# Optimization experiments

Hardware: AMD Instinct MI355X
Metric: run time of the kernel (lower is better)

## Reference

```python
import jax, jax.numpy as jnp
import numpy as np
from collections import deque

N, IN_DIM, H, B, L = 512, 64, 128, 256, 2
SOURCE = 105
E_UND = 2048


def _build_graph_and_masks():
    rng = np.random.default_rng(0)
    s = rng.integers(0, N, E_UND)
    d = rng.integers(0, N, E_UND)
    edge_index = np.stack([np.concatenate([s, d]), np.concatenate([d, s])]).astype(np.int32)
    # BFS depths from source (undirected)
    adj = [[] for _ in range(N)]
    for a, b in zip(edge_index[0], edge_index[1]):
        adj[int(a)].append(int(b))
    depths = np.full(N, np.inf)
    depths[SOURCE] = 0.0
    q = deque([SOURCE]); seen = {SOURCE}
    while q:
        u = q.popleft()
        for v in adj[u]:
            if v not in seen:
                seen.add(v); depths[v] = depths[u] + 1.0; q.append(v)
    finite = np.isfinite(depths)
    maxd = depths[finite].max() if finite.any() else 0.0
    depths[~finite] = maxd + 1.0
    adj_mask = np.zeros((N, N), np.float32)
    adj_mask[edge_index[0], edge_index[1]] = 1.0
    adj_mask[edge_index[1], edge_index[0]] = 1.0
    np.fill_diagonal(adj_mask, 1.0)
    direction_mask = (depths[None, :] <= depths[:, None]).astype(np.float32)
    # admittance_matrix is None -> uniform init, then masked
    initial_causal = (np.ones((N, N), np.float32) / N) * adj_mask * direction_mask
    return edge_index, adj_mask, direction_mask, initial_causal


def setup_inputs() -> dict:
    key = jax.random.key(0)
    ks = jax.random.split(key, 16)
    edge_index, adj_mask, direction_mask, initial_causal = _build_graph_and_masks()
    w = lambda k, shp: jax.random.normal(k, shp, jnp.float32) * 0.02
    return {
        'x': jax.random.normal(ks[0], (B, N, IN_DIM), jnp.float32),
        'edge_index': jnp.asarray(edge_index),
        'adj_mask': jnp.asarray(adj_mask),
        'direction_mask': jnp.asarray(direction_mask),
        'causal_logits': jnp.asarray(initial_causal),  # nn.Parameter init
        'W_in': w(ks[1], (IN_DIM, H)), 'b_in': jnp.zeros((H,), jnp.float32),
        'Wq': w(ks[2], (H, H)), 'bq': jnp.zeros((H,), jnp.float32),
        'Wk': w(ks[3], (H, H)), 'bk': jnp.zeros((H,), jnp.float32),
        'Wv': w(ks[4], (H, H)), 'bv': jnp.zeros((H,), jnp.float32),
        'gcn_W': w(ks[5], (L, H, H)), 'gcn_b': jnp.zeros((L, H), jnp.float32),
        'W_fuse': w(ks[6], (2 * H, H)), 'b_fuse': jnp.zeros((H,), jnp.float32),
        'ln_g': jnp.ones((H,), jnp.float32), 'ln_b': jnp.zeros((H,), jnp.float32),
    }


def reference(x, edge_index, adj_mask, direction_mask, causal_logits,
              W_in, b_in, Wq, bq, Wk, bk, Wv, bv,
              gcn_W, gcn_b, W_fuse, b_fuse, ln_g, ln_b):
    n = adj_mask.shape[0]
    h = jax.nn.relu(x @ W_in + b_in)                               # (B,N,H)

    # causal matrix: softmax over learned logits, physically masked, renormalized
    C = jax.nn.softmax(causal_logits, axis=-1) * adj_mask * direction_mask
    C = C / jnp.clip(C.sum(-1, keepdims=True), 1e-8)

    # masked causal attention
    Q = h @ Wq + bq; K = h @ Wk + bk; V = h @ Wv + bv
    scale = jnp.asarray(h.shape[-1] ** 0.5, h.dtype)
    attn = jax.nn.softmax(jnp.einsum('bnh,bmh->bnm', Q, K) / scale, axis=-1)
    attn = attn * C[None]
    attn = attn / (attn.sum(-1, keepdims=True) + 1e-8)
    h_causal = jnp.einsum('bnm,bmh->bnh', attn, V)

    # GCNConv stack (self-loops + symmetric norm; dropout is identity in eval)
    src = jnp.concatenate([edge_index[0], jnp.arange(n, dtype=edge_index.dtype)])
    dst = jnp.concatenate([edge_index[1], jnp.arange(n, dtype=edge_index.dtype)])
    deg = jnp.zeros((n,), h.dtype).at[dst].add(1.0)
    dinv = deg ** -0.5                                              # deg>=1 (self loops)
    norm = (dinv[src] * dinv[dst])[None, :, None]                   # (1,E+N,1)
    h_g = h
    for l in range(gcn_W.shape[0]):
        hW = h_g @ gcn_W[l]                                         # (B,N,H)
        msg = hW[:, src, :] * norm                                  # (B,E+N,H)
        h_g = jnp.zeros_like(hW).at[:, dst, :].add(msg) + gcn_b[l]
        h_g = jax.nn.relu(h_g)

    h_comb = jnp.concatenate([h_causal, h_g], axis=-1) @ W_fuse + b_fuse
    mu = h_comb.mean(-1, keepdims=True)
    var = ((h_comb - mu) ** 2).mean(-1, keepdims=True)
    out = (h_comb - mu) / jnp.sqrt(var + 1e-5) * ln_g + ln_b
    return out, C
```

## Files before the change

kernel.cpp:

```cpp
#include <hip/hip_runtime.h>
#include <hip/hip_bf16.h>
#include <math.h>

#define NN 512
#define HH 128
#define INDIM 64
#define BB 256
#define NE 4096
#define MROWS (BB*NN)
#define OUT0 (BB*NN*HH)

typedef __attribute__((ext_vector_type(8))) short short8v;
typedef __attribute__((ext_vector_type(4))) float float4v;

__device__ __forceinline__ unsigned short f2bf(float f) {
  unsigned u = __float_as_uint(f);
  unsigned r = (u + 0x7fffu + ((u >> 16) & 1u)) >> 16;
  return (unsigned short)r;
}
__device__ __forceinline__ float bf2f(unsigned short b) {
  return __uint_as_float(((unsigned)b) << 16);
}

__global__ __launch_bounds__(256) void k_causalC(
    const float* __restrict__ logits, const float* __restrict__ adj,
    const float* __restrict__ dir, float* __restrict__ Cout)
{
  const int row = blockIdx.x;
  const int t = threadIdx.x;
  __shared__ float red[256];
  const float* lrow = logits + (size_t)row * NN;
  float v0 = lrow[t], v1 = lrow[t + 256];
  float mx = fmaxf(v0, v1);
  red[t] = mx; __syncthreads();
  for (int s = 128; s > 0; s >>= 1) { if (t < s) red[t] = fmaxf(red[t], red[t + s]); __syncthreads(); }
  mx = red[0]; __syncthreads();
  float e0 = __expf(v0 - mx), e1 = __expf(v1 - mx);
  red[t] = e0 + e1; __syncthreads();
  for (int s = 128; s > 0; s >>= 1) { if (t < s) red[t] += red[t + s]; __syncthreads(); }
  float sumE = red[0]; __syncthreads();
  float m0 = adj[(size_t)row * NN + t] * dir[(size_t)row * NN + t];
  float m1 = adj[(size_t)row * NN + t + 256] * dir[(size_t)row * NN + t + 256];
  float me0 = e0 * m0, me1 = e1 * m1;
  red[t] = me0 + me1; __syncthreads();
  for (int s = 128; s > 0; s >>= 1) { if (t < s) red[t] += red[t + s]; __syncthreads(); }
  float sumME = red[0];
  float sm = sumME / sumE;
  float denom = fmaxf(sm, 1e-8f) * sumE;
  Cout[(size_t)row * NN + t]       = me0 / denom;
  Cout[(size_t)row * NN + t + 256] = me1 / denom;
}

__global__ __launch_bounds__(512) void k_csr(const int* __restrict__ ei,
                                             int* __restrict__ rp,
                                             int* __restrict__ ci,
                                             float* __restrict__ cw)
{
  __shared__ int scnt[512];
  __shared__ float sdinv[512];
  __shared__ int sval[512];
  __shared__ int scur[512];
  const int t = threadIdx.x;
  const int* src = ei;
  const int* dst = ei + NE;
  scnt[t] = 0;
  __syncthreads();
  for (int e = t; e < NE; e += 512) atomicAdd(&scnt[dst[e]], 1);
  __syncthreads();
  const int deg = scnt[t] + 1;
  sdinv[t] = rsqrtf((float)deg);
  sval[t] = deg;
  __syncthreads();
  for (int off = 1; off < 512; off <<= 1) {
    int add = (t >= off) ? sval[t - off] : 0;
    __syncthreads();
    sval[t] += add;
    __syncthreads();
  }
  const int excl = sval[t] - deg;
  rp[t] = excl;
  if (t == 511) rp[512] = excl + deg;
  ci[excl] = t;
  cw[excl] = sdinv[t] * sdinv[t];
  scur[t] = excl + 1;
  __syncthreads();
  for (int e = t; e < NE; e += 512) {
    int s = src[e], d = dst[e];
    int p = atomicAdd(&scur[d], 1);
    ci[p] = s;
    cw[p] = sdinv[s] * sdinv[d];
  }
}

__global__ __launch_bounds__(512) void k_ccsr(const int* __restrict__ ei,
                                              const float* __restrict__ Cmat,
                                              int* __restrict__ rp,
                                              int* __restrict__ ci,
                                              float* __restrict__ cw)
{
  __shared__ unsigned bm[512 * 16];
  __shared__ int cnt[512];
  __shared__ int sval[512];
  __shared__ int cur[512];
  const int t = threadIdx.x;
  const int* src = ei;
  const int* dst = ei + NE;
  for (int i = t; i < 512 * 16; i += 512) bm[i] = 0u;
  __syncthreads();
  bm[t * 16 + (t >> 5)] |= (1u << (t & 31));
  cnt[t] = 1;
  __syncthreads();
  for (int e = t; e < NE; e += 512) {
    int r = src[e], c = dst[e];
    if (Cmat[(size_t)r * NN + c] > 0.f) {
      unsigned bit = 1u << (c & 31);
      unsigned old = atomicOr(&bm[r * 16 + (c >> 5)], bit);
      if (!(old & bit)) atomicAdd(&cnt[r], 1);
    }
  }
  __syncthreads();
  const int myc = cnt[t];
  sval[t] = myc;
  __syncthreads();
  for (int off = 1; off < 512; off <<= 1) {
    int add = (t >= off) ? sval[t - off] : 0;
    __syncthreads();
    sval[t] += add;
    __syncthreads();
  }
  const int excl = sval[t] - myc;
  rp[t] = excl;
  if (t == 511) rp[512] = excl + myc;
  ci[excl] = t;
  cw[excl] = Cmat[(size_t)t * NN + t];
  cur[t] = excl + 1;
  bm[t * 16 + (t >> 5)] &= ~(1u << (t & 31));
  __syncthreads();
  for (int e = t; e < NE; e += 512) {
    int r = src[e], c = dst[e];
    if (Cmat[(size_t)r * NN + c] > 0.f) {
      unsigned bit = 1u << (c & 31);
      unsigned old = atomicAnd(&bm[r * 16 + (c >> 5)], ~bit);
      if (old & bit) {
        int p = atomicAdd(&cur[r], 1);
        ci[p] = c;
        cw[p] = Cmat[(size_t)r * NN + c];
      }
    }
  }
}

__device__ __forceinline__ void gcn_body(
    int bid, const unsigned short* __restrict__ hW,
    const int* __restrict__ rp, const int* __restrict__ ci,
    const float* __restrict__ cw, const float* __restrict__ bias,
    unsigned short* __restrict__ out, int OS, int OC0)
{
  const int i5 = bid >> 3;
  const int ng = i5 & 31;
  const int b = (bid & 7) * 32 + (i5 >> 5);
  const int t = threadIdx.x;
  const int node = ng * 16 + (t >> 4);
  const int f0 = (t & 15) * 8;

  float bcol[8];
  #pragma unroll
  for (int k = 0; k < 8; k++) bcol[k] = bias[f0 + k];

  const unsigned short* base = hW + (size_t)b * 512 * 128;
  const int beg = rp[node], end = rp[node + 1];
  float acc[8] = {0.f, 0.f, 0.f, 0.f, 0.f, 0.f, 0.f, 0.f};
  for (int j = beg; j < end; j++) {
    int s = ci[j];
    float w = cw[j];
    short8v v = *(const short8v*)&base[(size_t)s * 128 + f0];
    #pragma unroll
    for (int k = 0; k < 8; k++) acc[k] += w * bf2f((unsigned short)v[k]);
  }
  short8v o;
  #pragma unroll
  for (int k = 0; k < 8; k++) {
    float v = fmaxf(acc[k] + bcol[k], 0.f);
    o[k] = (short)f2bf(v);
  }
  *(short8v*)&out[((size_t)(b * 512 + node)) * OS + OC0 + f0] = o;
}

__global__ __launch_bounds__(256) void k_gcn(
    const unsigned short* __restrict__ hW,
    const int* __restrict__ rp, const int* __restrict__ ci,
    const float* __restrict__ cw, const float* __restrict__ bias,
    unsigned short* __restrict__ out, int OS, int OC0)
{
  gcn_body(blockIdx.x, hW, rp, ci, cw, bias, out, OS, OC0);
}

__device__ __forceinline__ void sattn_body(
    int bid, const unsigned short* __restrict__ Qbf,
    const unsigned short* __restrict__ Kbf, const unsigned short* __restrict__ Vbf,
    const int* __restrict__ rp, const int* __restrict__ ci,
    const float* __restrict__ cw, unsigned short* __restrict__ Ocb)
{
  const int i5 = bid >> 3;
  const int ng = i5 & 31;
  const int b = (bid & 7) * 32 + (i5 >> 5);
  const int t = threadIdx.x;
  const int node = ng * 16 + (t >> 4);
  const int f0 = (t & 15) * 8;
  const float scale = 0.088388347648318447f;

  const size_t rowq = ((size_t)(b * 512 + node)) * 128 + f0;
  short8v qv = *(const short8v*)&Qbf[rowq];
  float qf[8];
  #pragma unroll
  for (int k = 0; k < 8; k++) qf[k] = bf2f((unsigned short)qv[k]);

  const unsigned short* Kb = Kbf + (size_t)b * 512 * 128;
  const unsigned short* Vb = Vbf + (size_t)b * 512 * 128;
  const int beg = rp[node], end = rp[node + 1];
  float acc[8] = {0.f, 0.f, 0.f, 0.f, 0.f, 0.f, 0.f, 0.f};
  float sw = 0.f;
  int j = beg;
  float w0 = cw[j];
  int m = ci[j];
  short8v kv = *(const short8v*)&Kb[(size_t)m * 128 + f0];
  short8v vv = *(const short8v*)&Vb[(size_t)m * 128 + f0];
  for (; j < end; ) {
    const int jn = (j + 1 < end) ? j + 1 : j;
    const float w02 = cw[jn];
    const int m2 = ci[jn];
    short8v kv2 = *(const short8v*)&Kb[(size_t)m2 * 128 + f0];
    short8v vv2 = *(const short8v*)&Vb[(size_t)m2 * 128 + f0];
    float part = 0.f;
    #pragma unroll
    for (int k = 0; k < 8; k++) part += qf[k] * bf2f((unsigned short)kv[k]);
    part += __shfl_xor(part, 1);
    part += __shfl_xor(part, 2);
    part += __shfl_xor(part, 4);
    part += __shfl_xor(part, 8);
    float w = __expf(part * scale) * w0;
    sw += w;
    #pragma unroll
    for (int k = 0; k < 8; k++) acc[k] += w * bf2f((unsigned short)vv[k]);
    j++;
    w0 = w02; kv = kv2; vv = vv2;
  }
  float inv = 1.0f / sw;
  short8v o;
  #pragma unroll
  for (int k = 0; k < 8; k++) o[k] = (short)f2bf(acc[k] * inv);
  *(short8v*)&Ocb[((size_t)(b * 512 + node)) * 256 + f0] = o;
}

__global__ __launch_bounds__(256) void k_gs(
    const unsigned short* __restrict__ hW,
    const int* __restrict__ grp, const int* __restrict__ gci,
    const float* __restrict__ gcw, const float* __restrict__ gbias,
    const unsigned short* __restrict__ Qbf, const unsigned short* __restrict__ Kbf,
    const unsigned short* __restrict__ Vbf,
    const int* __restrict__ arp, const int* __restrict__ aci,
    const float* __restrict__ acw,
    unsigned short* __restrict__ Dout)
{
  if (blockIdx.x < 8192)
    gcn_body(blockIdx.x, hW, grp, gci, gcw, gbias, Dout, 256, 128);
  else
    sattn_body(blockIdx.x - 8192, Qbf, Kbf, Vbf, arp, aci, acw, Dout);
}

__global__ __launch_bounds__(256) void k_wt(
    const float* s0, const float* s1, const float* s2, const float* s3,
    const float* s4, const float* s5, const float* s6,
    unsigned short* d0, unsigned short* d1, unsigned short* d2, unsigned short* d3,
    unsigned short* d4, unsigned short* d5, unsigned short* d6)
{
  const float* srcs[7] = {s0, s1, s2, s3, s4, s5, s6};
  unsigned short* dsts[7] = {d0, d1, d2, d3, d4, d5, d6};
  const int Ks[7] = {64, 128, 128, 128, 128, 128, 256};
  const int j = blockIdx.x >> 3;
  const int nc = blockIdx.x & 7;
  const float* s = srcs[j];
  unsigned short* d = dsts[j];
  const int K = Ks[j];
  const int STRW = K + 8;
  const int n0 = nc * 16;
  __shared__ short tile[16 * 264];
  const int t = threadIdx.x;
  for (int i = t; i < K * 16; i += 256) {
    int k = i >> 4, nn = i & 15;
    tile[nn * STRW + k] = (short)f2bf(s[k * 128 + n0 + nn]);
  }
  __syncthreads();
  for (int i = t; i < K * 2; i += 256) {
    int nn = (i * 8) / K;
    int k  = (i * 8) % K;
    *(short8v*)&d[(size_t)(n0 + nn) * K + k] =
        *(const short8v*)&tile[nn * STRW + k];
  }
}

template<bool RELU>
__global__ __launch_bounds__(256) void k_wgemm(
    const unsigned short* __restrict__ Abf,
    const unsigned short* __restrict__ Wt,
    const float* __restrict__ bias,
    unsigned short* __restrict__ Out)
{
  constexpr int STR = 136;
  __shared__ short Ws[128 * STR];
  __shared__ short rep[4 * 2048];
  const int t = threadIdx.x;
  const int wave = t >> 6, lane = t & 63;
  const int l15 = lane & 15, quad = lane >> 4;
  short* rw = rep + wave * 2048;

  for (int i = t; i < 128 * 16; i += 256) {
    int n = i >> 4, seg = i & 15;
    *(short8v*)&Ws[n * STR + seg * 8] =
        *(const short8v*)&Wt[(size_t)n * 128 + seg * 8];
  }
  float bcol[8];
  #pragma unroll
  for (int nt = 0; nt < 8; nt++) bcol[nt] = bias ? bias[nt * 16 + l15] : 0.f;
  __syncthreads();

  const int nwaves = gridDim.x * 4;
  int tile = blockIdx.x * 4 + wave;
  short8v af[4], afn[4];
  if (tile < MROWS / 16) {
    #pragma unroll
    for (int dc = 0; dc < 4; dc++)
      af[dc] = *(const short8v*)&Abf[((size_t)(tile * 16 + l15)) * 128 + dc * 32 + quad * 8];
  }
  while (tile < MROWS / 16) {
    const int ntile = tile + nwaves;
    if (ntile < MROWS / 16) {
      #pragma unroll
      for (int dc = 0; dc < 4; dc++)
        afn[dc] = *(const short8v*)&Abf[((size_t)(ntile * 16 + l15)) * 128 + dc * 32 + quad * 8];
    }
    float4v acc[8];
    #pragma unroll
    for (int nt = 0; nt < 8; nt++) acc[nt] = (float4v){0.f, 0.f, 0.f, 0.f};
    #pragma unroll
    for (int k32 = 0; k32 < 4; k32++) {
      #pragma unroll
      for (int nt = 0; nt < 8; nt++) {
        short8v wf = *(const short8v*)&Ws[(nt * 16 + l15) * STR + k32 * 32 + quad * 8];
        acc[nt] = __builtin_amdgcn_mfma_f32_16x16x32_bf16(af[k32], wf, acc[nt], 0, 0, 0);
      }
    }
    #pragma unroll
    for (int nt = 0; nt < 8; nt++)
      #pragma unroll
      for (int r = 0; r < 4; r++) {
        float v = acc[nt][r] + bcol[nt];
        if (RELU) v = fmaxf(v, 0.f);
        rw[(quad * 4 + r) * 128 + nt * 16 + l15] = (short)f2bf(v);
      }
    asm volatile("s_waitcnt lgkmcnt(0)" ::: "memory");
    __builtin_amdgcn_sched_barrier(0);
    #pragma unroll
    for (int p = 0; p < 4; p++) {
      int row16 = (lane >> 4) + p * 4, seg = lane & 15;
      short8v vv = *(const short8v*)&rw[row16 * 128 + seg * 8];
      *(short8v*)&Out[((size_t)(tile * 16 + row16)) * 128 + seg * 8] = vv;
    }
    tile = ntile;
    #pragma unroll
    for (int dc = 0; dc < 4; dc++) af[dc] = afn[dc];
  }
}

#define GNT 4
template<int KD, bool RELU, bool BATCHW, int OMODE, bool AF32>
__global__ __launch_bounds__(256) void k_bgemm(
    const void* __restrict__ Ap, const unsigned short* __restrict__ Wt,
    const float* __restrict__ bias, void* __restrict__ Out, int OS,
    const float* __restrict__ lng, const float* __restrict__ lnb)
{
  constexpr int KCH = (KD < 128) ? KD : 128;
  constexpr int STR = KCH + 8;
  constexpr bool WONCE = (KD <= 128);
  constexpr int ASH = (64 * STR > 8192) ? 64 * STR : 8192;
  constexpr int TRIPS = KCH / 32;
  __shared__ short lds[ASH + 128 * STR];
  short* As = lds;
  short* Ws = lds + ASH;
  const unsigned short* Abf = (const unsigned short*)Ap;
  const float* Af = (const float*)Ap;
  const int t = threadIdx.x;
  const int wave = t >> 6, lane = t & 63;
  const int l15 = lane & 15, quad = lane >> 4;

  short8v ap[TRIPS];
  float4 fa[TRIPS], fb[TRIPS];

  auto LOADC = [&](int rb, int kc) {
    #pragma unroll
    for (int j = 0; j < TRIPS; j++) {
      int i = t + j * 256;
      int r = i / (KCH / 8), seg = i % (KCH / 8);
      if (AF32) {
        const float* sp = &Af[(size_t)(rb + r) * KD + kc + seg * 8];
        fa[j] = *(const float4*)sp;
        fb[j] = *(const float4*)(sp + 4);
      } else {
        int arow = BATCHW ? ((rb & 511) + r) : (rb + r);
        ap[j] = *(const short8v*)&Abf[(size_t)arow * KD + kc + seg * 8];
      }
    }
  };
  auto STOREC = [&]() {
    #pragma unroll
    for (int j = 0; j < TRIPS; j++) {
      int i = t + j * 256;
      int r = i / (KCH / 8), seg = i % (KCH / 8);
      if (AF32) {
        short8v pk;
        pk[0] = (short)f2bf(fa[j].x); pk[1] = (short)f2bf(fa[j].y);
        pk[2] = (short)f2bf(fa[j].z); pk[3] = (short)f2bf(fa[j].w);
        pk[4] = (short)f2bf(fb[j].x); pk[5] = (short)f2bf(fb[j].y);
        pk[6] = (short)f2bf(fb[j].z); pk[7] = (short)f2bf(fb[j].w);
        *(short8v*)&As[r * STR + seg * 8] = pk;
      } else {
        *(short8v*)&As[r * STR + seg * 8] = ap[j];
      }
    }
  };

  float bcol[8];
  #pragma unroll
  for (int nt = 0; nt < 8; nt++) bcol[nt] = bias ? bias[nt * 16 + l15] : 0.f;
  float gcol[8], bbcol[8];
  if (OMODE == 2) {
    #pragma unroll
    for (int nt = 0; nt < 8; nt++) { gcol[nt] = lng[nt * 16 + l15]; bbcol[nt] = lnb[nt * 16 + l15]; }
  }

  for (int g = blockIdx.x; g < (MROWS / 64) / GNT; g += gridDim.x) {
    if (WONCE) {
      const int b0 = (g * GNT * 64) >> 9;
      const unsigned short* Wb = BATCHW ? (Wt + (size_t)b0 * 128 * KD) : Wt;
      for (int i = t; i < 128 * (KCH / 8); i += 256) {
        int n = i / (KCH / 8), seg = i % (KCH / 8);
        *(short8v*)&Ws[n * STR + seg * 8] =
            *(const short8v*)&Wb[(size_t)n * KD + seg * 8];
      }
    }
    LOADC(g * GNT * 64, 0);
    for (int tt = 0; tt < GNT; tt++) {
      const int tile = g * GNT + tt;
      const int rowbase = tile * 64;
      const int b = rowbase >> 9;
      float4v acc[8];
      #pragma unroll
      for (int nt = 0; nt < 8; nt++) acc[nt] = (float4v){0.f, 0.f, 0.f, 0.f};

      for (int kc = 0; kc < KD; kc += KCH) {
        __syncthreads();
        STOREC();
        if (!WONCE) {
          const unsigned short* Wb = BATCHW ? (Wt + (size_t)b * 128 * KD) : Wt;
          for (int i = t; i < 128 * (KCH / 8); i += 256) {
            int n = i / (KCH / 8), seg = i % (KCH / 8);
            *(short8v*)&Ws[n * STR + seg * 8] =
                *(const short8v*)&Wb[(size_t)n * KD + kc + seg * 8];
          }
        }
        __syncthreads();
        {
          int nkc = kc + KCH, ntt = tt;
          if (nkc >= KD) { nkc = 0; ntt = tt + 1; }
          if (ntt < GNT) LOADC((g * GNT + ntt) * 64, nkc);
        }
        #pragma unroll
        for (int k32 = 0; k32 < KCH / 32; k32++) {
          short8v af = *(const short8v*)&As[(wave * 16 + l15) * STR + k32 * 32 + quad * 8];
          #pragma unroll
          for (int nt = 0; nt < 8; nt++) {
            short8v wf = *(const short8v*)&Ws[(nt * 16 + l15) * STR + k32 * 32 + quad * 8];
            acc[nt] = __builtin_amdgcn_mfma_f32_16x16x32_bf16(af, wf, acc[nt], 0, 0, 0);
          }
        }
      }

      __syncthreads();
      if (OMODE == 0) {
        short* rep = As + wave * 2048;
        #pragma unroll
        for (int nt = 0; nt < 8; nt++)
          #pragma unroll
          for (int r = 0; r < 4; r++) {
            float v = acc[nt][r] + bcol[nt];
            if (RELU) v = fmaxf(v, 0.f);
            rep[(quad * 4 + r) * 128 + nt * 16 + l15] = (short)f2bf(v);
          }
        __syncthreads();
        unsigned short* Ob = (unsigned short*)Out;
        #pragma unroll
        for (int p = 0; p < 4; p++) {
          int row16 = (lane >> 4) + p * 4, seg = lane & 15;
          short8v vv = *(const short8v*)&rep[row16 * 128 + seg * 8];
          *(short8v*)&Ob[(size_t)(rowbase + wave * 16 + row16) * OS + seg * 8] = vv;
        }
      } else if (OMODE == 1) {
        short* rep = As + wave * 2048;
        #pragma unroll
        for (int nt = 0; nt < 8; nt++)
          #pragma unroll
          for (int r = 0; r < 4; r++) {
            float v = acc[nt][r] + bcol[nt];
            if (RELU) v = fmaxf(v, 0.f);
            rep[(nt * 16 + l15) * 16 + quad * 4 + r] = (short)f2bf(v);
          }
        __syncthreads();
        unsigned short* Ob = (unsigned short*)Out;
        int node0 = (rowbase & 511) + wave * 16;
        #pragma unroll
        for (int p = 0; p < 4; p++) {
          int idx = p * 64 + lane, c = idx >> 1, half = idx & 1;
          short8v vv = *(const short8v*)&rep[c * 16 + half * 8];
          *(short8v*)&Ob[((size_t)(b * 128 + c)) * 512 + node0 + half * 8] = vv;
        }
      } else {
        float* repw = (float*)lds + wave * 2048;
        float vv[8][4];
        float s[4] = {0, 0, 0, 0}, ss[4] = {0, 0, 0, 0};
        #pragma unroll
        for (int nt = 0; nt < 8; nt++)
          #pragma unroll
          for (int r = 0; r < 4; r++) {
            float v = acc[nt][r] + bcol[nt];
            vv[nt][r] = v;
            s[r] += v; ss[r] += v * v;
          }
        #pragma unroll
        for (int r = 0; r < 4; r++) {
          s[r] += __shfl_xor(s[r], 1);  s[r] += __shfl_xor(s[r], 2);
          s[r] += __shfl_xor(s[r], 4);  s[r] += __shfl_xor(s[r], 8);
          ss[r] += __shfl_xor(ss[r], 1); ss[r] += __shfl_xor(ss[r], 2);
          ss[r] += __shfl_xor(ss[r], 4); ss[r] += __shfl_xor(ss[r], 8);
        }
        #pragma unroll
        for (int r = 0; r < 4; r++) {
          float mu = s[r] * (1.0f / 128.0f);
          float var = ss[r] * (1.0f / 128.0f) - mu * mu;
          float inv = rsqrtf(var + 1e-5f);
          #pragma unroll
          for (int nt = 0; nt < 8; nt++)
            repw[(quad * 4 + r) * 128 + nt * 16 + l15] =
                (vv[nt][r] - mu) * inv * gcol[nt] + bbcol[nt];
        }
        __syncthreads();
        float* Of = (float*)Out;
        #pragma unroll
        for (int p = 0; p < 8; p++) {
          int row16 = (lane >> 5) + p * 2, seg = lane & 31;
          float4 o = *(const float4*)&repw[row16 * 128 + seg * 4];
          *(float4*)&Of[(size_t)(rowbase + wave * 16 + row16) * 128 + seg * 4] = o;
        }
      }
    }
  }
}

__global__ __launch_bounds__(256) void k_hqkv4(
    const float* __restrict__ x,
    const unsigned short* __restrict__ Wint,
    const float* __restrict__ bin,
    const unsigned short* __restrict__ W0, const unsigned short* __restrict__ W1,
    const unsigned short* __restrict__ W2, const unsigned short* __restrict__ W3,
    const float* __restrict__ b1, const float* __restrict__ b2,
    const float* __restrict__ b3,
    unsigned short* __restrict__ O0, unsigned short* __restrict__ O1,
    unsigned short* __restrict__ O2, unsigned short* __restrict__ O3)
{
  constexpr int STR = 136;
  constexpr int RSTR = 136;
  __shared__ short Ws[128 * STR];
  __shared__ short rep[4 * 2304];
  const int t = threadIdx.x;
  const int wave = t >> 6, lane = t & 63;
  const int l15 = lane & 15, quad = lane >> 4;
  short* rw = rep + wave * 2304;

  const unsigned short* Wsrc[4] = {W0, W1, W2, W3};
  const float* Bsrc[4] = {nullptr, b1, b2, b3};
  unsigned short* Osrc[4] = {O0, O1, O2, O3};

  float bh[8];
  #pragma unroll
  for (int nt = 0; nt < 8; nt++) bh[nt] = bin[nt * 16 + l15];

  for (int g = blockIdx.x; g < (MROWS / 64) / GNT; g += gridDim.x) {
    short8v wif[2][8];
    #pragma unroll
    for (int k32 = 0; k32 < 2; k32++)
      #pragma unroll
      for (int nt = 0; nt < 8; nt++)
        wif[k32][nt] = *(const short8v*)&Wint[(size_t)(nt * 16 + l15) * 64 + k32 * 32 + quad * 8];

    short8v af_all[GNT][4];
    #pragma unroll
    for (int tt = 0; tt < GNT; tt++) {
      const int row0 = (g * GNT + tt) * 64 + wave * 16;
      const float* xp = &x[(size_t)(row0 + l15) * 64 + quad * 16];
      float4 fx0 = *(const float4*)(xp);
      float4 fx1 = *(const float4*)(xp + 4);
      float4 fx2 = *(const float4*)(xp + 8);
      float4 fx3 = *(const float4*)(xp + 12);
      short8v px0, px1;
      px0[0] = (short)f2bf(fx0.x); px0[1] = (short)f2bf(fx0.y);
      px0[2] = (short)f2bf(fx0.z); px0[3] = (short)f2bf(fx0.w);
      px0[4] = (short)f2bf(fx1.x); px0[5] = (short)f2bf(fx1.y);
      px0[6] = (short)f2bf(fx1.z); px0[7] = (short)f2bf(fx1.w);
      px1[0] = (short)f2bf(fx2.x); px1[1] = (short)f2bf(fx2.y);
      px1[2] = (short)f2bf(fx2.z); px1[3] = (short)f2bf(fx2.w);
      px1[4] = (short)f2bf(fx3.x); px1[5] = (short)f2bf(fx3.y);
      px1[6] = (short)f2bf(fx3.z); px1[7] = (short)f2bf(fx3.w);
      *(short8v*)&rw[l15 * 72 + quad * 16]     = px0;
      *(short8v*)&rw[l15 * 72 + quad * 16 + 8] = px1;
      asm volatile("s_waitcnt lgkmcnt(0)" ::: "memory");
      __builtin_amdgcn_sched_barrier(0);

      float4v hacc[8];
      #pragma unroll
      for (int nt = 0; nt < 8; nt++) hacc[nt] = (float4v){0.f, 0.f, 0.f, 0.f};
      #pragma unroll
      for (int k32 = 0; k32 < 2; k32++) {
        short8v ax = *(const short8v*)&rw[l15 * 72 + k32 * 32 + quad * 8];
        #pragma unroll
        for (int nt = 0; nt < 8; nt++)
          hacc[nt] = __builtin_amdgcn_mfma_f32_16x16x32_bf16(ax, wif[k32][nt], hacc[nt], 0, 0, 0);
      }
      #pragma unroll
      for (int nt = 0; nt < 8; nt++)
        #pragma unroll
        for (int r = 0; r < 4; r++) {
          float v = fmaxf(hacc[nt][r] + bh[nt], 0.f);
          rw[(quad * 4 + r) * RSTR + nt * 16 + l15] = (short)f2bf(v);
        }
      asm volatile("s_waitcnt lgkmcnt(0)" ::: "memory");
      __builtin_amdgcn_sched_barrier(0);
      #pragma unroll
      for (int dc = 0; dc < 4; dc++)
        af_all[tt][dc] = *(const short8v*)&rw[l15 * RSTR + dc * 32 + quad * 8];
    }

    #pragma unroll
    for (int s = 0; s < 4; s++) {
      __syncthreads();
      for (int i = t; i < 128 * 16; i += 256) {
        int n = i >> 4, seg = i & 15;
        *(short8v*)&Ws[n * STR + seg * 8] =
            *(const short8v*)&Wsrc[s][(size_t)n * 128 + seg * 8];
      }
      float bcol[8];
      #pragma unroll
      for (int nt = 0; nt < 8; nt++) bcol[nt] = Bsrc[s] ? Bsrc[s][nt * 16 + l15] : 0.f;
      __syncthreads();

      #pragma unroll
      for (int tt = 0; tt < GNT; tt++) {
        const int rowbase = (g * GNT + tt) * 64;
        float4v acc[8];
        #pragma unroll
        for (int nt = 0; nt < 8; nt++) acc[nt] = (float4v){0.f, 0.f, 0.f, 0.f};
        #pragma unroll
        for (int k32 = 0; k32 < 4; k32++) {
          #pragma unroll
          for (int nt = 0; nt < 8; nt++) {
            short8v wf = *(const short8v*)&Ws[(nt * 16 + l15) * STR + k32 * 32 + quad * 8];
            acc[nt] = __builtin_amdgcn_mfma_f32_16x16x32_bf16(af_all[tt][k32], wf, acc[nt], 0, 0, 0);
          }
        }
        #pragma unroll
        for (int nt = 0; nt < 8; nt++)
          #pragma unroll
          for (int r = 0; r < 4; r++) {
            float v = acc[nt][r] + bcol[nt];
            rw[(quad * 4 + r) * RSTR + nt * 16 + l15] = (short)f2bf(v);
          }
        asm volatile("s_waitcnt lgkmcnt(0)" ::: "memory");
        __builtin_amdgcn_sched_barrier(0);
        unsigned short* Ob = Osrc[s];
        #pragma unroll
        for (int p = 0; p < 4; p++) {
          int row16 = (lane >> 4) + p * 4, seg = lane & 15;
          short8v vv = *(const short8v*)&rw[row16 * RSTR + seg * 8];
          *(short8v*)&Ob[(size_t)(rowbase + wave * 16 + row16) * 128 + seg * 8] = vv;
        }
      }
    }
  }
}

extern "C" void kernel_launch(void* const* d_in, const int* in_sizes, int n_in,
                              void* d_out, int out_size, void* d_ws, size_t ws_size,
                              hipStream_t stream)
{
  const float* x     = (const float*)d_in[0];
  const int*   ei    = (const int*)d_in[1];
  const float* adj   = (const float*)d_in[2];
  const float* dmask = (const float*)d_in[3];
  const float* clog  = (const float*)d_in[4];
  const float* W_in  = (const float*)d_in[5];
  const float* b_in  = (const float*)d_in[6];
  const float* Wq    = (const float*)d_in[7];
  const float* bq    = (const float*)d_in[8];
  const float* Wk    = (const float*)d_in[9];
  const float* bk    = (const float*)d_in[10];
  const float* Wv    = (const float*)d_in[11];
  const float* bv    = (const float*)d_in[12];
  const float* gcnW  = (const float*)d_in[13];
  const float* gcnB  = (const float*)d_in[14];
  const float* Wf    = (const float*)d_in[15];
  const float* bf    = (const float*)d_in[16];
  const float* lng   = (const float*)d_in[17];
  const float* lnb   = (const float*)d_in[18];

  float* outp = (float*)d_out;
  float* Cmat = outp + OUT0;

  char* W = (char*)d_ws;
  const size_t SLOT = (size_t)MROWS * 128 * 2;
  unsigned short* A0 = (unsigned short*)(W);
  unsigned short* B0 = (unsigned short*)(W + SLOT);
  unsigned short* C0 = (unsigned short*)(W + 2 * SLOT);
  unsigned short* D0 = (unsigned short*)(W + 3 * SLOT);
  char* AUX = W + 5 * SLOT;
  int*   csr_rp = (int*)AUX;
  int*   csr_ci = csr_rp + 640;
  float* csr_cw = (float*)(csr_ci + 4608);
  int*   crp    = (int*)(AUX + 131072);
  int*   cci    = crp + 640;
  float* ccw    = (float*)(cci + 8192);
  unsigned short* WB    = (unsigned short*)(AUX + 512 * 512 * 4) + 512 * 512 * 2;
  unsigned short* W_int = WB;
  unsigned short* Wqt   = WB + 8192;
  unsigned short* Wkt   = Wqt + 16384;
  unsigned short* Wvt   = Wkt + 16384;
  unsigned short* G0t   = Wvt + 16384;
  unsigned short* G1t   = G0t + 16384;
  unsigned short* Wft   = G1t + 16384;

  unsigned short* Vbf = (unsigned short*)outp;
  unsigned short* E0  = Vbf + (size_t)MROWS * 128;

  k_causalC<<<512, 256, 0, stream>>>(clog, adj, dmask, Cmat);
  k_csr<<<1, 512, 0, stream>>>(ei, csr_rp, csr_ci, csr_cw);
  k_ccsr<<<1, 512, 0, stream>>>(ei, Cmat, crp, cci, ccw);
  k_wt<<<56, 256, 0, stream>>>(W_in, Wq, Wk, Wv, gcnW, gcnW + HH * HH, Wf,
                               W_int, Wqt, Wkt, Wvt, G0t, G1t, Wft);

  k_hqkv4<<<512, 256, 0, stream>>>(
      x, W_int, b_in, G0t, Wqt, Wkt, Wvt, bq, bk, bv, A0, C0, E0, Vbf);
  k_gcn<<<8192, 256, 0, stream>>>(A0, csr_rp, csr_ci, csr_cw, gcnB, B0, 128, 0);
  k_wgemm<false><<<768, 256, 0, stream>>>(B0, G1t, nullptr, A0);
  k_gs<<<16384, 256, 0, stream>>>(
      A0, csr_rp, csr_ci, csr_cw, gcnB + HH,
      C0, E0, Vbf, crp, cci, ccw, D0);
  k_bgemm<256, false, false, 2, false><<<512, 256, 0, stream>>>(
      D0, Wft, bf, outp, 128, lng, lnb);
}
```

Before: 392.8 us.

## Use 512-thread blocks for hqkv4 and wgemm, stage W_in in LDS

```diff
diff --git a/kernel.cpp b/kernel.cpp
--- a/kernel.cpp
+++ b/kernel.cpp
@@ -300,7 +300,7 @@
 }
 
 template<bool RELU>
-__global__ __launch_bounds__(256) void k_wgemm(
+__global__ __launch_bounds__(512) void k_wgemm(
     const unsigned short* __restrict__ Abf,
     const unsigned short* __restrict__ Wt,
     const float* __restrict__ bias,
@@ -308,13 +308,13 @@
 {
   constexpr int STR = 136;
   __shared__ short Ws[128 * STR];
-  __shared__ short rep[4 * 2048];
+  __shared__ short rep[8 * 2048];
   const int t = threadIdx.x;
   const int wave = t >> 6, lane = t & 63;
   const int l15 = lane & 15, quad = lane >> 4;
   short* rw = rep + wave * 2048;
 
-  for (int i = t; i < 128 * 16; i += 256) {
+  for (int i = t; i < 128 * 16; i += 512) {
     int n = i >> 4, seg = i & 15;
     *(short8v*)&Ws[n * STR + seg * 8] =
         *(const short8v*)&Wt[(size_t)n * 128 + seg * 8];
@@ -324,8 +324,8 @@
   for (int nt = 0; nt < 8; nt++) bcol[nt] = bias ? bias[nt * 16 + l15] : 0.f;
   __syncthreads();
 
-  const int nwaves = gridDim.x * 4;
-  int tile = blockIdx.x * 4 + wave;
+  const int nwaves = gridDim.x * 8;
+  int tile = blockIdx.x * 8 + wave;
   short8v af[4], afn[4];
   if (tile < MROWS / 16) {
     #pragma unroll
@@ -565,7 +565,7 @@
   }
 }
 
-__global__ __launch_bounds__(256) void k_hqkv4(
+__global__ __launch_bounds__(512) void k_hqkv4(
     const float* __restrict__ x,
     const unsigned short* __restrict__ Wint,
     const float* __restrict__ bin,
@@ -579,7 +579,7 @@
   constexpr int STR = 136;
   constexpr int RSTR = 136;
   __shared__ short Ws[128 * STR];
-  __shared__ short rep[4 * 2304];
+  __shared__ short rep[8 * 2304];
   const int t = threadIdx.x;
   const int wave = t >> 6, lane = t & 63;
   const int l15 = lane & 15, quad = lane >> 4;
@@ -593,18 +593,19 @@
   #pragma unroll
   for (int nt = 0; nt < 8; nt++) bh[nt] = bin[nt * 16 + l15];
 
-  for (int g = blockIdx.x; g < (MROWS / 64) / GNT; g += gridDim.x) {
-    short8v wif[2][8];
-    #pragma unroll
-    for (int k32 = 0; k32 < 2; k32++)
-      #pragma unroll
-      for (int nt = 0; nt < 8; nt++)
-        wif[k32][nt] = *(const short8v*)&Wint[(size_t)(nt * 16 + l15) * 64 + k32 * 32 + quad * 8];
-
-    short8v af_all[GNT][4];
-    #pragma unroll
-    for (int tt = 0; tt < GNT; tt++) {
-      const int row0 = (g * GNT + tt) * 64 + wave * 16;
+  for (int g = blockIdx.x; g < MROWS / 256; g += gridDim.x) {
+    __syncthreads();
+    for (int i = t; i < 128 * 8; i += 512) {
+      int n = i >> 3, seg = i & 7;
+      *(short8v*)&Ws[n * STR + seg * 8] =
+          *(const short8v*)&Wint[(size_t)n * 64 + seg * 8];
+    }
+    __syncthreads();
+
+    short8v af_all[2][4];
+    #pragma unroll
+    for (int tt = 0; tt < 2; tt++) {
+      const int row0 = (g * 2 + tt) * 128 + wave * 16;
       const float* xp = &x[(size_t)(row0 + l15) * 64 + quad * 16];
       float4 fx0 = *(const float4*)(xp);
       float4 fx1 = *(const float4*)(xp + 4);
@@ -631,8 +632,10 @@
       for (int k32 = 0; k32 < 2; k32++) {
         short8v ax = *(const short8v*)&rw[l15 * 72 + k32 * 32 + quad * 8];
         #pragma unroll
-        for (int nt = 0; nt < 8; nt++)
-          hacc[nt] = __builtin_amdgcn_mfma_f32_16x16x32_bf16(ax, wif[k32][nt], hacc[nt], 0, 0, 0);
+        for (int nt = 0; nt < 8; nt++) {
+          short8v wf = *(const short8v*)&Ws[(nt * 16 + l15) * STR + k32 * 32 + quad * 8];
+          hacc[nt] = __builtin_amdgcn_mfma_f32_16x16x32_bf16(ax, wf, hacc[nt], 0, 0, 0);
+        }
       }
       #pragma unroll
       for (int nt = 0; nt < 8; nt++)
@@ -651,7 +654,7 @@
     #pragma unroll
     for (int s = 0; s < 4; s++) {
       __syncthreads();
-      for (int i = t; i < 128 * 16; i += 256) {
+      for (int i = t; i < 128 * 16; i += 512) {
         int n = i >> 4, seg = i & 15;
         *(short8v*)&Ws[n * STR + seg * 8] =
             *(const short8v*)&Wsrc[s][(size_t)n * 128 + seg * 8];
@@ -662,8 +665,8 @@
       __syncthreads();
 
       #pragma unroll
-      for (int tt = 0; tt < GNT; tt++) {
-        const int rowbase = (g * GNT + tt) * 64;
+      for (int tt = 0; tt < 2; tt++) {
+        const int rowbase = (g * 2 + tt) * 128;
         float4v acc[8];
         #pragma unroll
         for (int nt = 0; nt < 8; nt++) acc[nt] = (float4v){0.f, 0.f, 0.f, 0.f};
@@ -754,10 +757,10 @@
   k_wt<<<56, 256, 0, stream>>>(W_in, Wq, Wk, Wv, gcnW, gcnW + HH * HH, Wf,
                                W_int, Wqt, Wkt, Wvt, G0t, G1t, Wft);
 
-  k_hqkv4<<<512, 256, 0, stream>>>(
+  k_hqkv4<<<512, 512, 0, stream>>>(
       x, W_int, b_in, G0t, Wqt, Wkt, Wvt, bq, bk, bv, A0, C0, E0, Vbf);
   k_gcn<<<8192, 256, 0, stream>>>(A0, csr_rp, csr_ci, csr_cw, gcnB, B0, 128, 0);
-  k_wgemm<false><<<768, 256, 0, stream>>>(B0, G1t, nullptr, A0);
+  k_wgemm<false><<<512, 512, 0, stream>>>(B0, G1t, nullptr, A0);
   k_gs<<<16384, 256, 0, stream>>>(
       A0, csr_rp, csr_ci, csr_cw, gcnB + HH,
       C0, E0, Vbf, crp, cci, ccw, D0);
```

After: 364.5 us. 7.2% less time.
